# Performance work log

Hardware: AMD Instinct MI355X
Metric: run time of the kernel (lower is better)

Reference implementation:

```python
import jax, jax.numpy as jnp
import numpy as np

K = 3           # kernel_size
PAD = 1         # padding
HEADS = 6
C = 192
CH = C // HEADS           # channels per head = 32
SCALE = CH ** (-0.5)
KK = K * K                # 9


def unfold3(x):
    # x: [N,C,H,W] -> [N,C,9,H,W] (im2col with k=3, pad=1, stride=1)
    N, c, H, W = x.shape
    xp = jnp.pad(x, ((0, 0), (0, 0), (PAD, PAD), (PAD, PAD)))
    return jnp.stack([xp[:, :, i:i + H, j:j + W] for i in range(K) for j in range(K)], axis=2)


def fold3(y):
    # y: [N,C,9,H,W] -> [N,C,H,W] (scatter-add inverse of unfold3)
    N, c, kk, H, W = y.shape
    out = jnp.zeros((N, c, H + 2 * PAD, W + 2 * PAD), dtype=y.dtype)
    idx = 0
    for i in range(K):
        for j in range(K):
            out = out.at[:, :, i:i + H, j:j + W].add(y[:, :, idx])
            idx += 1
    return out[:, :, PAD:PAD + H, PAD:PAD + W]


def setup_inputs() -> dict:
    key = jax.random.key(0)
    ks = jax.random.split(key, 6)
    N, H, W = 16, 56, 56
    s = 0.02
    return {
        "x": jax.random.normal(ks[0], (N, C, H, W), jnp.float32),
        "Wv": jax.random.normal(ks[1], (C, C), jnp.float32) * s,          # fc (no bias)
        "Wa": jax.random.normal(ks[2], (C, KK * KK * HEADS), jnp.float32) * s,  # fc_att weight
        "ba": jax.random.normal(ks[3], (KK * KK * HEADS,), jnp.float32) * s,
        "Wp": jax.random.normal(ks[4], (C, C), jnp.float32) * s,          # fc_proj weight
        "bp": jax.random.normal(ks[5], (C,), jnp.float32) * s,
    }


def reference(x, Wv, Wa, ba, Wp, bp):
    N, c, H, W = x.shape
    HW = H * W
    # value projection (pointwise linear over channels)
    v = jnp.einsum("nchw,cd->ndhw", x, Wv)
    # unfold values: [N,C,9,H,W] -> [N,heads,ch,9,HW] -> [N,heads,HW,9,ch]
    vu = unfold3(v).reshape(N, HEADS, CH, KK, HW).transpose(0, 1, 4, 3, 2)
    # attention logits from (avg-pooled, here identity since stride=1) input
    att = jnp.einsum("nchw,ck->nhwk", x, Wa) + ba       # [N,H,W,81*heads]
    att = att.reshape(N, HW, HEADS, KK, KK).transpose(0, 2, 1, 3, 4)  # [N,heads,HW,9,9]
    att = jax.nn.softmax(att * SCALE, axis=-1)          # dropout is identity at inference
    # apply per-position 9x9 attention to the 9 gathered neighbors
    out = jnp.einsum("nhpkl,nhplc->nhpkc", att, vu)      # [N,heads,HW,9,ch]
    # fold back: layout (heads, ch, kk) matches unfold layout (C, kk)
    out = out.transpose(0, 1, 4, 3, 2).reshape(N, c, KK, H, W)
    folded = fold3(out)                                  # [N,C,H,W]
    # output projection
    return jnp.einsum("nchw,cd->ndhw", folded, Wp) + bp[None, :, None, None]
```

## Files before the change

### kernel.cpp

```cpp
#include <hip/hip_runtime.h>
#include <hip/hip_bf16.h>
#include <math.h>

#define HW 3136
#define NPOS 50176
#define NC 192
#define NHEADS 6
#define IMG 56
#define NATT 486
#define ATT_SCALE 0.17677669529663687f

typedef __attribute__((ext_vector_type(8))) short short8;
typedef __attribute__((ext_vector_type(8))) unsigned short ushort8;
typedef __attribute__((ext_vector_type(4))) float float4v;
typedef __attribute__((ext_vector_type(4))) unsigned int uint4v;

__device__ __forceinline__ float bf2f(unsigned short u) {
    unsigned int x = ((unsigned int)u) << 16;
    return __builtin_bit_cast(float, x);
}
__device__ __forceinline__ float bf2f_lo(unsigned int u) {
    return __builtin_bit_cast(float, u << 16);
}
__device__ __forceinline__ float bf2f_hi(unsigned int u) {
    return __builtin_bit_cast(float, u & 0xffff0000u);
}
__device__ __forceinline__ unsigned short f2bf(float f) {
    __hip_bfloat16 h = __float2bfloat16(f);
    return __builtin_bit_cast(unsigned short, h);
}
__device__ __forceinline__ void gload_lds16(const void* g, void* l) {
    __builtin_amdgcn_global_load_lds((const __attribute__((address_space(1))) void*)g,
                                     (__attribute__((address_space(3))) void*)l, 16, 0, 0);
}

__global__ __launch_bounds__(256) void transpose_x(const float* __restrict__ x,
                                                   unsigned short* __restrict__ xt)
{
    __shared__ float tile[64][65];
    int bx = blockIdx.x;
    int n = (bx * 64) / HW;
    int hw0 = (bx * 64) % HW;
    int c0 = blockIdx.y * 64;
    int tl = threadIdx.x & 63, tg = threadIdx.x >> 6;
    const float* xn = x + (size_t)n * NC * HW;
#pragma unroll
    for (int i = 0; i < 16; ++i)
        tile[tg * 16 + i][tl] = xn[(size_t)(c0 + tg * 16 + i) * HW + hw0 + tl];
    __syncthreads();
    unsigned short* xp = xt + ((size_t)n * HW + hw0) * NC + c0;
#pragma unroll
    for (int i = 0; i < 16; ++i) {
        int hwr = tg * 16 + i;
        xp[(size_t)hwr * NC + tl] = f2bf(tile[tl][hwr]);
    }
}

__global__ __launch_bounds__(256) void prep_weights(
    const float* __restrict__ Wv, const float* __restrict__ Wa, const float* __restrict__ Wp,
    const float* __restrict__ ba,
    unsigned short* __restrict__ Wall, unsigned short* __restrict__ Wpt,
    float* __restrict__ ball)
{
    int idx = blockIdx.x * 256 + threadIdx.x;
    if (idx < 36864) {
        int d = idx / 192, k = idx - d * 192;
        Wpt[idx] = f2bf(Wp[(size_t)k * NC + d]);
    }
    if (idx < 147456) {
        int d = idx / 192, k = idx - d * 192;
        unsigned short val;
        float bv = 0.f;
        if (d < 192) {
            val = f2bf(Wv[(size_t)k * NC + d]);
        } else {
            int dp = d - 192;
            int head = dp / 96, rr = dp - head * 96;
            int k9 = rr / 10, l = rr - k9 * 10;
            bool valid = (k9 < 9) && (l < 9);
            int src = head * 81 + k9 * 9 + l;
            val = valid ? f2bf(Wa[(size_t)k * NATT + src]) : (unsigned short)0;
            bv = valid ? ba[src] : 0.f;
        }
        Wall[idx] = val;
        if (k == 0) ball[d] = bv;
    }
}

__global__ __launch_bounds__(512, 4) void gemm_big(
    const unsigned short* __restrict__ A, const unsigned short* __restrict__ W,
    const float* __restrict__ ball,
    unsigned short* __restrict__ Vo, unsigned short* __restrict__ ATo)
{
    __shared__ __align__(16) unsigned short As[2][4096];
    __shared__ __align__(16) unsigned short Bs[2][4096];
    int t = threadIdx.x, lane = t & 63, wave = t >> 6;
    int bi = blockIdx.x;
    int slot = bi >> 3;
    int q6 = slot / 6;
    int rr_ = (bi & 7) + 8 * q6;
    int cc_ = slot - 6 * q6;
    int col0 = cc_ * 128, row0 = rr_ * 128;
    int fr = lane & 15, fq = lane >> 4;
    int wm = (wave >> 2) * 64, wn = (wave & 3) * 32;
    const char* Ab = (const char*)A;
    const char* Wb = (const char*)W;

    float4v acc[4][2] = {};

#define STAGE_BIG(buf, k0)                                                         \
    {                                                                              \
        gload_lds16(Ab + (size_t)(row0 + wave * 16 + (lane >> 2)) * 384 +          \
                        (k0) * 2 + (lane & 3) * 16,                                \
                    (char*)As[buf] + wave * 1024);                                 \
        gload_lds16(Wb + (size_t)(col0 + wave * 16 + (lane >> 2)) * 384 +          \
                        (k0) * 2 + (lane & 3) * 16,                                \
                    (char*)Bs[buf] + wave * 1024);                                 \
    }

    STAGE_BIG(0, 0);
    for (int s = 0; s < 6; ++s) {
        if (s < 5) {
            STAGE_BIG((s + 1) & 1, (s + 1) * 32);
            asm volatile("s_waitcnt vmcnt(2)\n\ts_barrier" ::: "memory");
        } else {
            asm volatile("s_waitcnt vmcnt(0)\n\ts_barrier" ::: "memory");
        }
        int buf = s & 1;
        short8 af[4], bf[2];
#pragma unroll
        for (int mi = 0; mi < 4; ++mi)
            af[mi] = *(const short8*)((const char*)As[buf] + (wm + mi * 16 + fr) * 64 + fq * 16);
#pragma unroll
        for (int ni = 0; ni < 2; ++ni)
            bf[ni] = *(const short8*)((const char*)Bs[buf] + (wn + ni * 16 + fr) * 64 + fq * 16);
        asm volatile("s_waitcnt lgkmcnt(0)\n\ts_barrier" ::: "memory");
#pragma unroll
        for (int mi = 0; mi < 4; ++mi)
#pragma unroll
            for (int ni = 0; ni < 2; ++ni)
                acc[mi][ni] = __builtin_amdgcn_mfma_f32_16x16x32_bf16(
                    af[mi], bf[ni], acc[mi][ni], 0, 0, 0);
    }

#pragma unroll
    for (int ni = 0; ni < 2; ++ni) {
        int col = col0 + wn + ni * 16 + fr;
        float b = ball[col];
        unsigned short* bptr;
        size_t rstr;
        bool valid;
        if (col < 192) {
            int hd = col >> 5, ch = col & 31;
            bptr = Vo + ((size_t)hd * NPOS) * 32 + ch;
            rstr = 32;
            valid = true;
        } else {
            int dp = col - 192;
            int hd = dp / 96, rr = dp - hd * 96;
            int k9 = rr / 10, l = rr - k9 * 10;
            valid = (k9 < 9);
            bptr = ATo + ((size_t)(hd * 9 + (k9 < 9 ? k9 : 8)) * NPOS) * 10 + l;
            rstr = 10;
        }
#pragma unroll
        for (int mi = 0; mi < 4; ++mi) {
            int row = row0 + wm + mi * 16 + fq * 4;
#pragma unroll
            for (int r = 0; r < 4; ++r) {
                unsigned short val = f2bf(acc[mi][ni][r] + b);
                if (valid) bptr[(size_t)(row + r) * rstr] = val;
            }
        }
    }
#undef STAGE_BIG
}

__global__ __launch_bounds__(256) void gemm_small(
    const unsigned short* __restrict__ A,
    const unsigned short* __restrict__ B,
    const float* __restrict__ bias, float* __restrict__ out)
{
    __shared__ __align__(16) unsigned short As[2][2048];
    __shared__ __align__(16) unsigned short Bs[2][8192];
    int t = threadIdx.x, lane = t & 63, wave = t >> 6;
    int n0 = blockIdx.x * 256, m0 = blockIdx.y * 64;
    int fr = lane & 15, fq = lane >> 4;
    int srow = lane >> 2, soff = (lane & 3) * 16;
    const char* Ab = (const char*)A;
    const char* Bb = (const char*)B;

    float4v acc[4][4] = {};

#define STAGE_SMALL(buf, k0)                                                      \
    {                                                                             \
        gload_lds16(Ab + (size_t)(m0 + wave * 16 + srow) * 384 + (k0)*2 + soff,   \
                    (char*)As[buf] + wave * 1024);                                \
        _Pragma("unroll")                                                         \
        for (int i = 0; i < 4; ++i) {                                             \
            int j = wave * 4 + i;                                                 \
            gload_lds16(Bb + (size_t)(n0 + j * 16 + srow) * 384 + (k0)*2 + soff,  \
                        (char*)Bs[buf] + j * 1024);                               \
        }                                                                         \
    }

    STAGE_SMALL(0, 0);
    for (int s = 0; s < 6; ++s) {
        if (s < 5) {
            STAGE_SMALL((s + 1) & 1, (s + 1) * 32);
            asm volatile("s_waitcnt vmcnt(5)\n\ts_barrier" ::: "memory");
        } else {
            asm volatile("s_waitcnt vmcnt(0)\n\ts_barrier" ::: "memory");
        }
        int buf = s & 1;
        short8 af[4], bf[4];
#pragma unroll
        for (int mi = 0; mi < 4; ++mi)
            af[mi] = *(const short8*)((const char*)As[buf] + (mi * 16 + fr) * 64 + fq * 16);
#pragma unroll
        for (int ni = 0; ni < 4; ++ni)
            bf[ni] = *(const short8*)((const char*)Bs[buf] + (wave * 64 + ni * 16 + fr) * 64 + fq * 16);
        asm volatile("s_waitcnt lgkmcnt(0)\n\ts_barrier" ::: "memory");
#pragma unroll
        for (int mi = 0; mi < 4; ++mi)
#pragma unroll
            for (int ni = 0; ni < 4; ++ni)
                acc[mi][ni] = __builtin_amdgcn_mfma_f32_16x16x32_bf16(
                    af[mi], bf[ni], acc[mi][ni], 0, 0, 0);
    }

#pragma unroll
    for (int ni = 0; ni < 4; ++ni) {
        int n = n0 + wave * 64 + ni * 16 + fr;
        int img = n / HW, phw = n - img * HW;
        float* op = out + (size_t)img * (NC * HW) + phw;
#pragma unroll
        for (int mi = 0; mi < 4; ++mi) {
            int m = m0 + mi * 16 + fq * 4;
#pragma unroll
            for (int r = 0; r < 4; ++r)
                op[(size_t)(m + r) * HW] = acc[mi][ni][r] + bias[m + r];
        }
    }
#undef STAGE_SMALL
}

__global__ __launch_bounds__(256, 4) void fused_att_agg(
    const unsigned short* __restrict__ V, const unsigned short* __restrict__ AT,
    unsigned short* __restrict__ fold)
{
    __shared__ __align__(16) char vt[4 * 434 * 16];
    int t = threadIdx.x;
    int bid = blockIdx.x;
    int head = bid % NHEADS; int tmp = bid / NHEADS;
    int tcol = tmp & 1; tmp >>= 1;
    int trow = tmp % 7; int img = tmp / 7;
    int h0 = trow * 8, w0 = tcol * 28;

    const unsigned short* Vh = V + (size_t)head * NPOS * 32;
    ushort8 stg[6];
#pragma unroll
    for (int i = 0; i < 6; ++i) {
        int u = i * 256 + t;
        int slot = u >> 2, q = u & 3;
        int vrow = slot >> 5, vcol = slot & 31;
        int hh = h0 - 2 + vrow, ww = w0 - 2 + vcol;
        bool ok = (hh >= 0) & (hh < IMG) & (ww >= 0) & (ww < IMG);
        int hc = min(max(hh, 0), IMG - 1);
        int wcl = min(max(ww, 0), IMG - 1);
        ushort8 val = *(const ushort8*)(Vh + (size_t)(img * HW + hc * IMG + wcl) * 32 + q * 8);
        if (!ok) val = (ushort8){};
        stg[i] = val;
    }

    int ph = t / 28, pw = t - (t / 28) * 28;
    int h = h0 + ph, w = w0 + pw;
    float wc[25];
#pragma unroll
    for (int d = 0; d < 25; ++d) wc[d] = 0.f;
    if (t < 224) {
        int head9 = head * 9;
#pragma unroll
        for (int k = 0; k < 9; ++k) {
            const int oky = k / 3 - 1, okx = k % 3 - 1;
            int hh = h - oky, ww = w - okx;
            bool ok = (hh >= 0) & (hh < IMG) & (ww >= 0) & (ww < IMG);
            int hc = min(max(hh, 0), IMG - 1);
            int wcl = min(max(ww, 0), IMG - 1);
            size_t nidx = (size_t)img * HW + hc * IMG + wcl;
            const unsigned int* ap32 =
                (const unsigned int*)(AT + ((size_t)(head9 + k) * NPOS + nidx) * 10);
            unsigned int u0 = ap32[0], u1 = ap32[1], u2 = ap32[2], u3 = ap32[3], u4 = ap32[4];
            float a[9] = { bf2f_lo(u0), bf2f_hi(u0), bf2f_lo(u1), bf2f_hi(u1),
                           bf2f_lo(u2), bf2f_hi(u2), bf2f_lo(u3), bf2f_hi(u3),
                           bf2f_lo(u4) };
            float m = -1e30f;
#pragma unroll
            for (int l = 0; l < 9; ++l) m = fmaxf(m, a[l]);
            float s = 0.f;
#pragma unroll
            for (int l = 0; l < 9; ++l) {
                a[l] = __expf((a[l] - m) * ATT_SCALE);
                s += a[l];
            }
            float g = ok ? (1.f / s) : 0.f;
#pragma unroll
            for (int l = 0; l < 9; ++l) {
                const int dy = (l / 3 - 1) - oky + 2;
                const int dx = (l % 3 - 1) - okx + 2;
                wc[dy * 5 + dx] += a[l] * g;
            }
        }
    }

#pragma unroll
    for (int i = 0; i < 6; ++i) {
        int u = i * 256 + t;
        int slot = u >> 2, q = u & 3;
        int vrow = slot >> 5, vcol = slot & 31;
        *(ushort8*)(vt + q * (434 * 16) + (vrow * 36 + vcol) * 16) = stg[i];
    }
    __syncthreads();

    if (t < 224) {
        int base = (ph * 36 + pw) * 16;
        int pos = img * HW + h * IMG + w;
        unsigned short* fo = fold + (size_t)pos * NC + head * 32;
#pragma unroll
        for (int q = 0; q < 4; ++q) {
            const char* vq = vt + q * (434 * 16) + base;
            float acc[8];
#pragma unroll
            for (int j = 0; j < 8; ++j) acc[j] = 0.f;
#pragma unroll
            for (int d = 0; d < 25; ++d) {
                const int dy = d / 5, dx = d % 5;
                float wf = wc[d];
                uint4v vv = *(const uint4v*)(vq + (dy * 36 + dx) * 16);
#pragma unroll
                for (int z = 0; z < 4; ++z) {
                    acc[2 * z]     += wf * bf2f_lo(vv[z]);
                    acc[2 * z + 1] += wf * bf2f_hi(vv[z]);
                }
            }
            ushort8 ov;
#pragma unroll
            for (int j = 0; j < 8; ++j) ov[j] = f2bf(acc[j]);
            *(ushort8*)(fo + q * 8) = ov;
        }
    }
}

extern "C" void kernel_launch(void* const* d_in, const int* in_sizes, int n_in,
                              void* d_out, int out_size, void* d_ws, size_t ws_size,
                              hipStream_t stream)
{
    const float* x  = (const float*)d_in[0];
    const float* Wv = (const float*)d_in[1];
    const float* Wa = (const float*)d_in[2];
    const float* ba = (const float*)d_in[3];
    const float* Wp = (const float*)d_in[4];
    const float* bp = (const float*)d_in[5];
    float* out = (float*)d_out;

    unsigned short* xt   = (unsigned short*)d_ws;
    unsigned short* V    = xt + 9633792;
    unsigned short* AT   = V + 9633792;
    unsigned short* Wall = AT + 27095040;
    unsigned short* Wpt  = Wall + 147456;
    float*          ball = (float*)(Wpt + 36864);
    unsigned short* foldb = xt;

    dim3 blk(256);
    prep_weights<<<576, blk, 0, stream>>>(Wv, Wa, Wp, ba, Wall, Wpt, ball);
    transpose_x<<<dim3(784, 3), blk, 0, stream>>>(x, xt);
    gemm_big<<<2352, dim3(512), 0, stream>>>(xt, Wall, ball, V, AT);
    fused_att_agg<<<1344, blk, 0, stream>>>(V, AT, foldb);
    gemm_small<<<dim3(196, 3), blk, 0, stream>>>(Wpt, foldb, bp, out);
}
```

Before: 183.4 us.

## Triple-buffer big GEMM staging and XOR-swizzle LDS tiles in both GEMMs

The large projection GEMM moves from a double-buffered to a triple-buffered LDS pipeline that prefetches two k-steps ahead, with the vmcnt waits adjusted to match. Both GEMMs now XOR-swizzle the 16-byte chunk position when global data is written into LDS, and read fragments back through the same swizzle, to cut LDS bank conflicts on the fragment loads. The extra buffer raises LDS use per block in the big GEMM, which may lower occupancy under its 4-blocks-per-CU launch bound. These GEMMs are only part of the total pipeline time.

```diff
diff --git a/kernel.cpp b/kernel.cpp
--- a/kernel.cpp
+++ b/kernel.cpp
@@ -92,8 +92,8 @@
     const float* __restrict__ ball,
     unsigned short* __restrict__ Vo, unsigned short* __restrict__ ATo)
 {
-    __shared__ __align__(16) unsigned short As[2][4096];
-    __shared__ __align__(16) unsigned short Bs[2][4096];
+    __shared__ __align__(16) unsigned short As[3][4096];
+    __shared__ __align__(16) unsigned short Bs[3][4096];
     int t = threadIdx.x, lane = t & 63, wave = t >> 6;
     int bi = blockIdx.x;
     int slot = bi >> 3;
@@ -103,6 +103,9 @@
     int col0 = cc_ * 128, row0 = rr_ * 128;
     int fr = lane & 15, fq = lane >> 4;
     int wm = (wave >> 2) * 64, wn = (wave & 3) * 32;
+    int srow = lane >> 2;
+    int sg = ((lane & 3) ^ ((lane >> 3) & 3)) * 16;
+    int rc = (fq ^ ((fr >> 1) & 3)) * 16;
     const char* Ab = (const char*)A;
     const char* Wb = (const char*)W;
 
@@ -110,30 +113,32 @@
 
 #define STAGE_BIG(buf, k0)                                                         \
     {                                                                              \
-        gload_lds16(Ab + (size_t)(row0 + wave * 16 + (lane >> 2)) * 384 +          \
-                        (k0) * 2 + (lane & 3) * 16,                                \
+        gload_lds16(Ab + (size_t)(row0 + wave * 16 + srow) * 384 + (k0) * 2 + sg,  \
                     (char*)As[buf] + wave * 1024);                                 \
-        gload_lds16(Wb + (size_t)(col0 + wave * 16 + (lane >> 2)) * 384 +          \
-                        (k0) * 2 + (lane & 3) * 16,                                \
+        gload_lds16(Wb + (size_t)(col0 + wave * 16 + srow) * 384 + (k0) * 2 + sg,  \
                     (char*)Bs[buf] + wave * 1024);                                 \
     }
 
     STAGE_BIG(0, 0);
+    STAGE_BIG(1, 32);
+#pragma unroll
     for (int s = 0; s < 6; ++s) {
-        if (s < 5) {
-            STAGE_BIG((s + 1) & 1, (s + 1) * 32);
+        int buf = s % 3;
+        if (s < 4) {
+            STAGE_BIG((s + 2) % 3, (s + 2) * 32);
+            asm volatile("s_waitcnt vmcnt(4)\n\ts_barrier" ::: "memory");
+        } else if (s == 4) {
             asm volatile("s_waitcnt vmcnt(2)\n\ts_barrier" ::: "memory");
         } else {
             asm volatile("s_waitcnt vmcnt(0)\n\ts_barrier" ::: "memory");
         }
-        int buf = s & 1;
         short8 af[4], bf[2];
 #pragma unroll
         for (int mi = 0; mi < 4; ++mi)
-            af[mi] = *(const short8*)((const char*)As[buf] + (wm + mi * 16 + fr) * 64 + fq * 16);
+            af[mi] = *(const short8*)((const char*)As[buf] + (wm + mi * 16 + fr) * 64 + rc);
 #pragma unroll
         for (int ni = 0; ni < 2; ++ni)
-            bf[ni] = *(const short8*)((const char*)Bs[buf] + (wn + ni * 16 + fr) * 64 + fq * 16);
+            bf[ni] = *(const short8*)((const char*)Bs[buf] + (wn + ni * 16 + fr) * 64 + rc);
         asm volatile("s_waitcnt lgkmcnt(0)\n\ts_barrier" ::: "memory");
 #pragma unroll
         for (int mi = 0; mi < 4; ++mi)
@@ -186,7 +191,9 @@
     int t = threadIdx.x, lane = t & 63, wave = t >> 6;
     int n0 = blockIdx.x * 256, m0 = blockIdx.y * 64;
     int fr = lane & 15, fq = lane >> 4;
-    int srow = lane >> 2, soff = (lane & 3) * 16;
+    int srow = lane >> 2;
+    int sg = ((lane & 3) ^ ((lane >> 3) & 3)) * 16;
+    int rc = (fq ^ ((fr >> 1) & 3)) * 16;
     const char* Ab = (const char*)A;
     const char* Bb = (const char*)B;
 
@@ -194,12 +201,12 @@
 
 #define STAGE_SMALL(buf, k0)                                                      \
     {                                                                             \
-        gload_lds16(Ab + (size_t)(m0 + wave * 16 + srow) * 384 + (k0)*2 + soff,   \
+        gload_lds16(Ab + (size_t)(m0 + wave * 16 + srow) * 384 + (k0)*2 + sg,     \
                     (char*)As[buf] + wave * 1024);                                \
         _Pragma("unroll")                                                         \
         for (int i = 0; i < 4; ++i) {                                             \
             int j = wave * 4 + i;                                                 \
-            gload_lds16(Bb + (size_t)(n0 + j * 16 + srow) * 384 + (k0)*2 + soff,  \
+            gload_lds16(Bb + (size_t)(n0 + j * 16 + srow) * 384 + (k0)*2 + sg,    \
                         (char*)Bs[buf] + j * 1024);                               \
         }                                                                         \
     }
@@ -216,10 +223,10 @@
         short8 af[4], bf[4];
 #pragma unroll
         for (int mi = 0; mi < 4; ++mi)
-            af[mi] = *(const short8*)((const char*)As[buf] + (mi * 16 + fr) * 64 + fq * 16);
+            af[mi] = *(const short8*)((const char*)As[buf] + (mi * 16 + fr) * 64 + rc);
 #pragma unroll
         for (int ni = 0; ni < 4; ++ni)
-            bf[ni] = *(const short8*)((const char*)Bs[buf] + (wave * 64 + ni * 16 + fr) * 64 + fq * 16);
+            bf[ni] = *(const short8*)((const char*)Bs[buf] + (wave * 64 + ni * 16 + fr) * 64 + rc);
         asm volatile("s_waitcnt lgkmcnt(0)\n\ts_barrier" ::: "memory");
 #pragma unroll
         for (int mi = 0; mi < 4; ++mi)
```

Result: no change. 182.9 us (-0.3%).
